# Kernel optimization log

Measured on AMD Instinct MI355X. Metric: run time of the kernel, lower is better.

Reference implementation:

```python
import jax, jax.numpy as jnp
import numpy as np

N_HEADS = 16
EMB_DIM = 1024
HEAD_DIM = EMB_DIM // N_HEADS


def setup_inputs() -> dict:
    key = jax.random.key(0)
    k1, k2, k3, k4, k5 = jax.random.split(key, 5)
    s = 1.0 / np.sqrt(EMB_DIM)
    return {
        "attn_in": jax.random.normal(k1, (4, 2048, EMB_DIM), dtype=jnp.float32),
        "W_qkv": jax.random.uniform(k2, (EMB_DIM, 3 * EMB_DIM), jnp.float32, -s, s),
        "b_qkv": jax.random.uniform(k3, (3 * EMB_DIM,), jnp.float32, -s, s),
        "W_out": jax.random.uniform(k4, (EMB_DIM, EMB_DIM), jnp.float32, -s, s),
        "b_out": jax.random.uniform(k5, (EMB_DIM,), jnp.float32, -s, s),
    }


def reference(attn_in, W_qkv, b_qkv, W_out, b_out):
    N, L, E = attn_in.shape
    qkv = attn_in @ W_qkv + b_qkv                      # [N, L, 3E]
    q, k, v = jnp.split(qkv, 3, axis=-1)
    # [N, L, E] -> [N, H, L, D]
    def heads(x):
        return x.reshape(N, L, N_HEADS, HEAD_DIM).transpose(0, 2, 1, 3)
    q, k, v = heads(q), heads(k), heads(v)
    scale = 1.0 / np.sqrt(HEAD_DIM)
    scores = jnp.einsum('nhqd,nhkd->nhqk', q, k) * scale   # [N, H, L, L]
    attn = jax.nn.softmax(scores, axis=-1)
    o = jnp.einsum('nhqk,nhkd->nhqd', attn, v)             # [N, H, L, D]
    o = o.transpose(0, 2, 1, 3).reshape(N, L, E)
    return o @ W_out + b_out
```

## Files before the change

kernel.cpp:

```cpp
#include <hip/hip_runtime.h>

typedef __attribute__((ext_vector_type(8))) short short8;
typedef __attribute__((ext_vector_type(4))) float f32x4;
typedef __attribute__((ext_vector_type(16))) float f32x16;

#define MFMA16(A,B,C) __builtin_amdgcn_mfma_f32_16x16x32_bf16(A,B,C,0,0,0)
#define MFMA32(A,B,C) __builtin_amdgcn_mfma_f32_32x32x16_bf16(A,B,C,0,0,0)

__device__ __forceinline__ short f2bf(float f){
  union { float f; unsigned int u; } v; v.f = f;
  unsigned int u = v.u;
  unsigned int r = (u + 0x7fffu + ((u >> 16) & 1u)) >> 16;
  return (short)r;
}

__device__ __forceinline__ unsigned pk2bf_hu(float x, float y){
  unsigned a = __builtin_bit_cast(unsigned, x) + 0x8000u;
  unsigned b = __builtin_bit_cast(unsigned, y) + 0x8000u;
  return __builtin_amdgcn_perm(b, a, 0x07060302u);
}

typedef const __attribute__((address_space(1))) void* gptr_t;
typedef __attribute__((address_space(3))) void* lptr_t;

__device__ __forceinline__ void gload16(const short* g, short* l){
  __builtin_amdgcn_global_load_lds((gptr_t)g, (lptr_t)l, 16, 0, 0);
}


__global__ __launch_bounds__(256) void cvt_x_kernel(const float* __restrict__ x,
                                                    short* __restrict__ xb){
  const size_t i = (size_t)blockIdx.x * 256 + threadIdx.x;
  const float4* p = (const float4*)x + i * 2;
  float4 a = p[0], b = p[1];
  short8 o;
  o[0]=f2bf(a.x); o[1]=f2bf(a.y); o[2]=f2bf(a.z); o[3]=f2bf(a.w);
  o[4]=f2bf(b.x); o[5]=f2bf(b.y); o[6]=f2bf(b.z); o[7]=f2bf(b.w);
  *(short8*)(xb + i * 8) = o;
}

__global__ __launch_bounds__(256) void cvt_t_kernel(const float* __restrict__ src,
                                                    short* __restrict__ dst,
                                                    int R, int C){
  __shared__ float tile[32][33];
  const int tx = threadIdx.x, ty = threadIdx.y;
  const int c0 = blockIdx.x * 32, r0 = blockIdx.y * 32;
  #pragma unroll
  for (int i = 0; i < 32; i += 8)
    tile[ty + i][tx] = src[(size_t)(r0 + ty + i) * C + c0 + tx];
  __syncthreads();
  #pragma unroll
  for (int i = 0; i < 32; i += 8)
    dst[(size_t)(c0 + ty + i) * R + r0 + tx] = f2bf(tile[tx][ty + i]);
}


template<int EPI>
__global__ __launch_bounds__(256, 4) void gemm_bt(
    const short* __restrict__ A, const short* __restrict__ BT,
    const float* __restrict__ bias,
    float* __restrict__ Cf,
    short* __restrict__ q_ws, short* __restrict__ k_ws, short* __restrict__ vt_ws)
{
  __shared__ __align__(16) short As[4096];
  __shared__ __align__(16) short Bs[4096];
  const int tid = threadIdx.x;
  const int bn = blockIdx.x, bm = blockIdx.y;
  const int lane = tid & 63, wid = tid >> 6;
  const int wr = wid >> 1, wc = wid & 1;
  const int r = lane & 15, g = lane >> 4;

  f32x4 acc[4][4] = {};

  const short* ag = A  + (size_t)(bm * 128 + (tid >> 2)) * 1024 + (tid & 3) * 8;
  const short* bg = BT + (size_t)(bn * 128 + (tid >> 2)) * 1024 + (tid & 3) * 8;
  short* asd = &As[tid * 8];
  short* bsd = &Bs[tid * 8];

  for (int kk = 0; kk < 32; ++kk){
    gload16(ag + kk * 32,             asd);
    gload16(ag + kk * 32 + 64 * 1024, asd + 2048);
    gload16(bg + kk * 32,             bsd);
    gload16(bg + kk * 32 + 64 * 1024, bsd + 2048);
    asm volatile("s_waitcnt vmcnt(0)" ::: "memory");
    __syncthreads();
    short8 a[4], b[4];
    #pragma unroll
    for (int mf = 0; mf < 4; ++mf)
      a[mf] = *(const short8*)&As[(wr * 64 + mf * 16 + r) * 32 + g * 8];
    #pragma unroll
    for (int nf = 0; nf < 4; ++nf)
      b[nf] = *(const short8*)&Bs[(wc * 64 + nf * 16 + r) * 32 + g * 8];
    #pragma unroll
    for (int mf = 0; mf < 4; ++mf)
      #pragma unroll
      for (int nf = 0; nf < 4; ++nf)
        acc[mf][nf] = MFMA16(a[mf], b[nf], acc[mf][nf]);
    __syncthreads();
  }

  if (EPI == 0){
    #pragma unroll
    for (int nf = 0; nf < 4; ++nf){
      const int c = bn * 128 + wc * 64 + nf * 16 + r;
      const float bv = bias[c];
      const int type = c >> 10;
      const int h = (c & 1023) >> 6, d = c & 63;
      const float mul = (type == 0) ? 0.18033688011112042f : 1.0f;
      #pragma unroll
      for (int mf = 0; mf < 4; ++mf){
        const int row0 = bm * 128 + wr * 64 + mf * 16 + g * 4;
        const int nb = row0 >> 11, l0 = row0 & 2047;
        f32x4 v = acc[mf][nf];
        if (type == 2){
          short4 pk;
          pk.x = f2bf(v[0] + bv); pk.y = f2bf(v[1] + bv);
          pk.z = f2bf(v[2] + bv); pk.w = f2bf(v[3] + bv);
          const int head = nb * 16 + h;
          *(short4*)&vt_ws[(((size_t)head * 32 + (l0 >> 6)) * 64 + d) * 64 + (l0 & 63)] = pk;
        } else {
          short* dst = (type == 0) ? q_ws : k_ws;
          const size_t base = ((size_t)(nb * 16 + h) * 2048 + l0) * 64 + d;
          #pragma unroll
          for (int j = 0; j < 4; ++j)
            dst[base + (size_t)j * 64] = f2bf((v[j] + bv) * mul);
        }
      }
    }
  } else {
    #pragma unroll
    for (int nf = 0; nf < 4; ++nf){
      const int c = bn * 128 + wc * 64 + nf * 16 + r;
      const float bv = bias[c];
      #pragma unroll
      for (int mf = 0; mf < 4; ++mf){
        const int row0 = bm * 128 + wr * 64 + mf * 16 + g * 4;
        f32x4 v = acc[mf][nf];
        #pragma unroll
        for (int j = 0; j < 4; ++j)
          Cf[(size_t)(row0 + j) * 1024 + c] = v[j] + bv;
      }
    }
  }
}


__global__ __launch_bounds__(512, 4) void attn_kernel(
    const short* __restrict__ qw, const short* __restrict__ kw,
    const short* __restrict__ vtw, short* __restrict__ ow)
{
  __shared__ __align__(16) short Ks[4][4096];
  __shared__ __align__(16) short Vs[4][4096];

  const int id = blockIdx.x;
  const int xcd = id & 7, j2 = id >> 3;
  const int nh = xcd * 8 + (j2 & 7);
  const int qt = j2 >> 3;
  const int tid = threadIdx.x;
  const int lane = tid & 63, w = tid >> 6;
  const int l31 = lane & 31, hi = lane >> 5, w7 = lane & 7;

  const size_t hoff = (size_t)nh * 2048 * 64;
  const short* kh = kw + hoff;
  const short* vh = vtw + hoff;

  const int srow = tid >> 3, schunk = tid & 7;
  const int scw = (schunk ^ (srow & 7)) * 8;
  const short* ksrc = kh + srow * 64 + scw;
  const short* vsrc = vh + srow * 64 + scw;

  unsigned aoffh[2][4];
  #pragma unroll
  for (int T = 0; T < 2; ++T)
    #pragma unroll
    for (int s = 0; s < 4; ++s)
      aoffh[T][s] = (unsigned)((l31 + 32 * T) * 64 + (((2 * s + hi) ^ w7) * 8));

  const int qrow0 = qt * 256 + w * 32;
  short8 qfr[4];
  #pragma unroll
  for (int s = 0; s < 4; ++s)
    qfr[s] = *(const short8*)(qw + hoff + (size_t)(qrow0 + l31) * 64 + s * 16 + hi * 8);

  f32x16 oa0 = {}, oa1 = {}, lacc = {};
  short8 onesB;
  #pragma unroll
  for (int i = 0; i < 8; ++i) onesB[i] = (short)0x3F80;

  auto compute = [&](const short* Kb, const short* Vb){
    f32x16 ss0, ss1;
    __builtin_amdgcn_s_setprio(1);
    {
      const f32x16 zz = {};
      ss0 = MFMA32(*(const short8*)&Kb[aoffh[0][0]], qfr[0], zz);
      ss1 = MFMA32(*(const short8*)&Kb[aoffh[1][0]], qfr[0], zz);
    }
    #pragma unroll
    for (int s = 1; s < 4; ++s){
      ss0 = MFMA32(*(const short8*)&Kb[aoffh[0][s]], qfr[s], ss0);
      ss1 = MFMA32(*(const short8*)&Kb[aoffh[1][s]], qfr[s], ss1);
    }
    __builtin_amdgcn_s_setprio(0);

    unsigned u0[8], u1[8];
    #pragma unroll
    for (int m = 0; m < 8; ++m){
      u0[m] = pk2bf_hu(__builtin_amdgcn_exp2f(ss0[2 * m]),
                       __builtin_amdgcn_exp2f(ss0[2 * m + 1]));
      u1[m] = pk2bf_hu(__builtin_amdgcn_exp2f(ss1[2 * m]),
                       __builtin_amdgcn_exp2f(ss1[2 * m + 1]));
    }

    short8 pa[4];
    #pragma unroll
    for (int s = 0; s < 4; ++s){
      const int sg = (s & 1) * 4;
      unsigned a0 = (s < 2) ? u0[sg + 0] : u1[sg + 0];
      unsigned a1 = (s < 2) ? u0[sg + 1] : u1[sg + 1];
      unsigned a2 = (s < 2) ? u0[sg + 2] : u1[sg + 2];
      unsigned a3 = (s < 2) ? u0[sg + 3] : u1[sg + 3];
      auto r02 = __builtin_amdgcn_permlane32_swap(a0, a2, false, false);
      auto r13 = __builtin_amdgcn_permlane32_swap(a1, a3, false, false);
      union { unsigned q[4]; short8 s8; } cv;
      cv.q[0] = (unsigned)r02[0]; cv.q[1] = (unsigned)r13[0];
      cv.q[2] = (unsigned)r02[1]; cv.q[3] = (unsigned)r13[1];
      pa[s] = cv.s8;
    }

    __builtin_amdgcn_s_setprio(1);
    #pragma unroll
    for (int s = 0; s < 4; ++s){
      oa0  = MFMA32(pa[s], *(const short8*)&Vb[aoffh[0][s]], oa0);
      oa1  = MFMA32(pa[s], *(const short8*)&Vb[aoffh[1][s]], oa1);
      lacc = MFMA32(pa[s], onesB, lacc);
    }
    __builtin_amdgcn_s_setprio(0);
  };

  gload16(ksrc,        &Ks[0][tid * 8]);
  gload16(vsrc,        &Vs[0][tid * 8]);
  gload16(ksrc + 4096, &Ks[1][tid * 8]);
  gload16(vsrc + 4096, &Vs[1][tid * 8]);

  for (int p = 0; p < 8; ++p){
    const int t0 = p * 4;
    asm volatile("s_waitcnt vmcnt(0)" ::: "memory");
    asm volatile("s_barrier" ::: "memory");
    gload16(ksrc + (t0 + 2) * 4096, &Ks[2][tid * 8]);
    gload16(vsrc + (t0 + 2) * 4096, &Vs[2][tid * 8]);
    gload16(ksrc + (t0 + 3) * 4096, &Ks[3][tid * 8]);
    gload16(vsrc + (t0 + 3) * 4096, &Vs[3][tid * 8]);
    compute(&Ks[0][0], &Vs[0][0]);
    compute(&Ks[1][0], &Vs[1][0]);
    asm volatile("s_waitcnt vmcnt(0)" ::: "memory");
    asm volatile("s_barrier" ::: "memory");
    {
      const int ts0 = (t0 + 4) & 31;
      const int ts1 = (t0 + 5) & 31;
      gload16(ksrc + ts0 * 4096, &Ks[0][tid * 8]);
      gload16(vsrc + ts0 * 4096, &Vs[0][tid * 8]);
      gload16(ksrc + ts1 * 4096, &Ks[1][tid * 8]);
      gload16(vsrc + ts1 * 4096, &Vs[1][tid * 8]);
    }
    compute(&Ks[2][0], &Vs[2][0]);
    compute(&Ks[3][0], &Vs[3][0]);
  }

  const int n = nh >> 4, h = nh & 15;
  #pragma unroll
  for (int j = 0; j < 16; ++j){
    const float inv = 1.0f / lacc[j];
    const int qr = (j & 3) + 8 * (j >> 2) + 4 * hi;
    const size_t base = ((size_t)n * 2048 + qrow0 + qr) * 1024 + h * 64 + l31;
    ow[base]      = f2bf(oa0[j] * inv);
    ow[base + 32] = f2bf(oa1[j] * inv);
  }
}


extern "C" void kernel_launch(void* const* d_in, const int* in_sizes, int n_in,
                              void* d_out, int out_size, void* d_ws, size_t ws_size,
                              hipStream_t stream){
  const float* attn_in = (const float*)d_in[0];
  const float* W_qkv   = (const float*)d_in[1];
  const float* b_qkv   = (const float*)d_in[2];
  const float* W_out   = (const float*)d_in[3];
  const float* b_out   = (const float*)d_in[4];
  float* out = (float*)d_out;

  char* ws = (char*)d_ws;
  short* xb    = (short*)(ws);
  short* wqT   = (short*)(ws + 16777216);
  short* woT   = (short*)(ws + 23068672);
  short* q_ws  = (short*)(ws + 25165824);
  short* k_ws  = (short*)(ws + 41943040);
  short* vt_ws = (short*)(ws + 58720256);
  short* o_ws  = (short*)(ws + 75497472);

  cvt_x_kernel<<<4096, 256, 0, stream>>>(attn_in, xb);
  cvt_t_kernel<<<dim3(96, 32), dim3(32, 8), 0, stream>>>(W_qkv, wqT, 1024, 3072);
  cvt_t_kernel<<<dim3(32, 32), dim3(32, 8), 0, stream>>>(W_out, woT, 1024, 1024);
  gemm_bt<0><<<dim3(24, 64), 256, 0, stream>>>(xb, wqT, b_qkv, nullptr, q_ws, k_ws, vt_ws);
  attn_kernel<<<512, 512, 0, stream>>>(q_ws, k_ws, vt_ws, o_ws);
  gemm_bt<1><<<dim3(8, 64), 256, 0, stream>>>(o_ws, woT, b_out, out, nullptr, nullptr, nullptr);
}
```

Before: 187.3 us.

## Double GEMM K-tile to 64 and XOR-swizzle LDS layout

The projection GEMM now stages a 64-wide K slice per iteration instead of 32, halving the number of load/wait/barrier rounds over K. The LDS tile is laid out with an XOR swizzle on 16-byte chunks so that the fragment reads for the MFMAs avoid bank conflicts. LDS use per block doubles, which may lower occupancy under the 4-blocks launch bound. Loads remain synchronous with a full wait before compute.

```diff
diff --git a/kernel.cpp b/kernel.cpp
--- a/kernel.cpp
+++ b/kernel.cpp
@@ -62,8 +62,8 @@
     float* __restrict__ Cf,
     short* __restrict__ q_ws, short* __restrict__ k_ws, short* __restrict__ vt_ws)
 {
-  __shared__ __align__(16) short As[4096];
-  __shared__ __align__(16) short Bs[4096];
+  __shared__ __align__(16) short As[8192];
+  __shared__ __align__(16) short Bs[8192];
   const int tid = threadIdx.x;
   const int bn = blockIdx.x, bm = blockIdx.y;
   const int lane = tid & 63, wid = tid >> 6;
@@ -72,30 +72,42 @@
 
   f32x4 acc[4][4] = {};
 
-  const short* ag = A  + (size_t)(bm * 128 + (tid >> 2)) * 1024 + (tid & 3) * 8;
-  const short* bg = BT + (size_t)(bn * 128 + (tid >> 2)) * 1024 + (tid & 3) * 8;
-  short* asd = &As[tid * 8];
-  short* bsd = &Bs[tid * 8];
-
-  for (int kk = 0; kk < 32; ++kk){
-    gload16(ag + kk * 32,             asd);
-    gload16(ag + kk * 32 + 64 * 1024, asd + 2048);
-    gload16(bg + kk * 32,             bsd);
-    gload16(bg + kk * 32 + 64 * 1024, bsd + 2048);
+  const int srow_lo = tid >> 3;
+  const int sc8 = ((tid & 7) ^ (srow_lo & 7)) * 8;
+  const short* agb = A  + (size_t)(bm * 128 + srow_lo) * 1024 + sc8;
+  const short* bgb = BT + (size_t)(bn * 128 + srow_lo) * 1024 + sc8;
+
+  auto stage = [&](int kk){
+    #pragma unroll
+    for (int j = 0; j < 4; ++j){
+      gload16(agb + (size_t)j * 32 * 1024 + kk * 64, &As[j * 2048 + tid * 8]);
+      gload16(bgb + (size_t)j * 32 * 1024 + kk * 64, &Bs[j * 2048 + tid * 8]);
+    }
+  };
+
+  for (int kk = 0; kk < 16; ++kk){
+    stage(kk);
     asm volatile("s_waitcnt vmcnt(0)" ::: "memory");
     __syncthreads();
-    short8 a[4], b[4];
-    #pragma unroll
-    for (int mf = 0; mf < 4; ++mf)
-      a[mf] = *(const short8*)&As[(wr * 64 + mf * 16 + r) * 32 + g * 8];
-    #pragma unroll
-    for (int nf = 0; nf < 4; ++nf)
-      b[nf] = *(const short8*)&Bs[(wc * 64 + nf * 16 + r) * 32 + g * 8];
-    #pragma unroll
-    for (int mf = 0; mf < 4; ++mf)
-      #pragma unroll
-      for (int nf = 0; nf < 4; ++nf)
-        acc[mf][nf] = MFMA16(a[mf], b[nf], acc[mf][nf]);
+    #pragma unroll
+    for (int ks = 0; ks < 2; ++ks){
+      short8 a[4], b[4];
+      #pragma unroll
+      for (int mf = 0; mf < 4; ++mf){
+        const int row = wr * 64 + mf * 16 + r;
+        a[mf] = *(const short8*)&As[row * 64 + (((ks * 4 + g) ^ (r & 7)) * 8)];
+      }
+      #pragma unroll
+      for (int nf = 0; nf < 4; ++nf){
+        const int row = wc * 64 + nf * 16 + r;
+        b[nf] = *(const short8*)&Bs[row * 64 + (((ks * 4 + g) ^ (r & 7)) * 8)];
+      }
+      #pragma unroll
+      for (int mf = 0; mf < 4; ++mf)
+        #pragma unroll
+        for (int nf = 0; nf < 4; ++nf)
+          acc[mf][nf] = MFMA16(a[mf], b[nf], acc[mf][nf]);
+    }
     __syncthreads();
   }
 
```

After: 169.3 us. -9.6%, faster.
